# Performance work log

Measured on AMD Instinct MI355X. Metric: run time of the kernel, lower is better.

## Reference

```python
import jax, jax.numpy as jnp
import numpy as np

D = 1024   # embedding_dim
H = 16     # head_num
DH = D // H
STD = 0.02


def setup_inputs() -> dict:
    key = jax.random.key(0)
    ks = jax.random.split(key, 8)
    B, S = 16, 2048
    inp = {
        "hidden_states": jax.random.normal(ks[0], (B, S, D), dtype=jnp.float32),
        "attention_mask": jnp.zeros((B, 1, S), dtype=jnp.float32),
        # nn.Linear params, stored as [in, out] for direct matmul
        "Wq": jax.random.normal(ks[1], (D, D), dtype=jnp.float32) * STD,
        "bq": jnp.zeros((D,), dtype=jnp.float32),
        "Wqa": jax.random.normal(ks[2], (D, H), dtype=jnp.float32) * STD,
        "bqa": jnp.zeros((H,), dtype=jnp.float32),
        "Wk": jax.random.normal(ks[3], (D, D), dtype=jnp.float32) * STD,
        "bk": jnp.zeros((D,), dtype=jnp.float32),
        "Wka": jax.random.normal(ks[4], (D, H), dtype=jnp.float32) * STD,
        "bka": jnp.zeros((H,), dtype=jnp.float32),
        "Wt": jax.random.normal(ks[5], (D, D), dtype=jnp.float32) * STD,
        "bt": jnp.zeros((D,), dtype=jnp.float32),
    }
    return inp


def reference(hidden_states, attention_mask, Wq, bq, Wqa, bqa, Wk, bk, Wka, bka, Wt, bt):
    B, S, _ = hidden_states.shape
    scale = 1.0 / np.sqrt(DH).astype(np.float32)

    mixed_q = hidden_states @ Wq + bq          # [B,S,D]
    mixed_k = hidden_states @ Wk + bk          # [B,S,D]

    # per-head query pooling scores: [B,S,H] -> [B,H,S]
    q_score = jnp.transpose(mixed_q @ Wqa + bqa, (0, 2, 1)) * scale + attention_mask
    q_weight = jax.nn.softmax(q_score, axis=-1)                 # [B,H,S]

    q_layer = mixed_q.reshape(B, S, H, DH).transpose(0, 2, 1, 3)  # [B,H,S,dh]
    pooled_q = jnp.einsum('bhs,bhsd->bhd', q_weight, q_layer)     # [B,H,dh]
    pooled_q_flat = pooled_q.reshape(B, 1, D)                     # [B,1,D] (head-major)

    # elementwise modulate keys with pooled query (broadcast, no repeat)
    mixed_qk = mixed_k * pooled_q_flat                            # [B,S,D]

    qk_score = jnp.transpose(mixed_qk @ Wka + bka, (0, 2, 1)) * scale + attention_mask
    qk_weight = jax.nn.softmax(qk_score, axis=-1)                 # [B,H,S]

    k_layer = mixed_qk.reshape(B, S, H, DH).transpose(0, 2, 1, 3)  # [B,H,S,dh]
    pooled_k = jnp.einsum('bhs,bhsd->bhd', qk_weight, k_layer)     # [B,H,dh]

    weighted = pooled_k[:, :, None, :] * q_layer                   # [B,H,S,dh]
    weighted = weighted.transpose(0, 2, 1, 3).reshape(B, S, D)     # [B,S,D]

    return weighted @ Wt + bt + mixed_q
```

## Files before the change

### kernel.cpp

```cpp
#include <hip/hip_runtime.h>
#include <hip/hip_bf16.h>
#include <stdint.h>

#define D_ 1024
#define H_ 16
#define DH_ 64
#define S_ 2048
#define B_ 16
static constexpr float SCALE = 0.125f;

typedef __bf16 bf16_t;
typedef __bf16 bf16x8 __attribute__((ext_vector_type(8)));
typedef __bf16 bf16x4 __attribute__((ext_vector_type(4)));
typedef float  f32x4  __attribute__((ext_vector_type(4)));

__device__ __forceinline__ void llds16(const void* g, void* l) {
  __builtin_amdgcn_global_load_lds(
      (const __attribute__((address_space(1))) void*)g,
      (__attribute__((address_space(3))) void*)l, 16, 0, 0);
}

__global__ __launch_bounds__(256)
void prep_all(const float* __restrict__ Wq, const float* __restrict__ Wk,
              const float* __restrict__ Wt, const float* __restrict__ Wqa,
              const float* __restrict__ Wka, const float* __restrict__ hs,
              bf16_t* __restrict__ WqT, bf16_t* __restrict__ WkT,
              bf16_t* __restrict__ WtT, bf16_t* __restrict__ WqaT,
              bf16_t* __restrict__ WkaT, bf16_t* __restrict__ hsb) {
  __shared__ bf16_t t[64][65];
  const int z = blockIdx.z;
  const int tid = threadIdx.x;
  if (z < 3) {
    const float* src = (z == 0) ? Wq : (z == 1) ? Wk : Wt;
    bf16_t* dst      = (z == 0) ? WqT : (z == 1) ? WkT : WtT;
    const int n0 = blockIdx.x * 64, k0 = blockIdx.y * 64;
    const int r = tid >> 4, c4 = (tid & 15) * 4;
#pragma unroll
    for (int p = 0; p < 4; ++p) {
      int row = p * 16 + r;
      f32x4 f = *(const f32x4*)&src[(size_t)(k0 + row) * 1024 + n0 + c4];
#pragma unroll
      for (int i = 0; i < 4; ++i) t[row][c4 + i] = (bf16_t)f[i];
    }
    __syncthreads();
#pragma unroll
    for (int p = 0; p < 4; ++p) {
      int row = p * 16 + r;
      bf16x4 v;
#pragma unroll
      for (int i = 0; i < 4; ++i) v[i] = t[c4 + i][row];
      *(bf16x4*)&dst[(size_t)(n0 + row) * 1024 + k0 + c4] = v;
    }
  } else if (z == 3) {
    int g = (blockIdx.y * 16 + blockIdx.x) * 256 + tid;
    if (g < 2048) {
      const float* src = (g < 1024) ? Wqa : Wka;
      bf16_t* dst      = (g < 1024) ? WqaT : WkaT;
      int k = g & 1023;
#pragma unroll
      for (int h = 0; h < H_; ++h) dst[h * 1024 + k] = (bf16_t)src[k * H_ + h];
    }
  } else {
    const int slice = z - 4;
    const int fb = blockIdx.y * 16 + blockIdx.x;
    const size_t tbase = ((size_t)slice * 256 + fb) * 256 + tid;
#pragma unroll
    for (int i = 0; i < 4; ++i) {
      size_t e = (tbase + (size_t)i * 1048576) * 8;
      f32x4 a = *(const f32x4*)&hs[e];
      f32x4 b = *(const f32x4*)&hs[e + 4];
      bf16x8 o;
#pragma unroll
      for (int j = 0; j < 4; ++j) { o[j] = (bf16_t)a[j]; o[4 + j] = (bf16_t)b[j]; }
      *(bf16x8*)&hsb[e] = o;
    }
  }
}

__global__ __launch_bounds__(256, 2)
void gemm_qk(const bf16_t* __restrict__ A, const bf16_t* __restrict__ WqT,
             const bf16_t* __restrict__ WkT, const float* __restrict__ bq,
             const float* __restrict__ bk, bf16_t* __restrict__ mq,
             bf16_t* __restrict__ mk) {
  constexpr int K = 1024, N = 1024;
  __shared__ __align__(16) bf16_t lA[128 * 32];
  __shared__ __align__(16) bf16_t lB[128 * 32];
  __shared__ __align__(16) float est[4][16 * 68];
  const int tid = threadIdx.x;
  const int lane = tid & 63, wid = tid >> 6;
  const int wr = wid >> 1, wc = wid & 1;

  const int wgid = (blockIdx.x & 7) * 512 + (blockIdx.x >> 3);
  const int m0 = (wgid >> 4) * 128;
  const int nsel = wgid & 15;
  const int n0 = (nsel & 7) * 128;
  const bf16_t* BT = (nsel < 8) ? WqT : WkT;
  const float* bias = (nsel < 8) ? bq : bk;
  bf16_t* Cout = (nsel < 8) ? mq : mk;

  const int ar = lane & 15;
  const int kq = lane >> 4;

  int rowc[2], colc[2], dstoff[2];
#pragma unroll
  for (int j = 0; j < 2; ++j) {
    int c = j * 256 + tid;
    int row = c >> 2, s = c & 3;
    rowc[j] = row;
    colc[j] = (((s - (row >> 1)) & 3) << 3);
    dstoff[j] = c * 8;
  }

  f32x4 acc[4][4] = {};

  for (int k0 = 0; k0 < K; k0 += 32) {
#pragma unroll
    for (int j = 0; j < 2; ++j) {
      llds16(BT + (size_t)(n0 + rowc[j]) * K + k0 + colc[j], lB + dstoff[j]);
      llds16(A + (size_t)(m0 + rowc[j]) * K + k0 + colc[j], lA + dstoff[j]);
    }
    __syncthreads();
    bf16x8 af[4], bg[4];
#pragma unroll
    for (int m = 0; m < 4; ++m) {
      int r = wr * 64 + m * 16 + ar;
      af[m] = *(const bf16x8*)&lA[r * 32 + (((kq + (r >> 1)) & 3) << 3)];
    }
#pragma unroll
    for (int n = 0; n < 4; ++n) {
      int r = wc * 64 + n * 16 + ar;
      bg[n] = *(const bf16x8*)&lB[r * 32 + (((kq + (r >> 1)) & 3) << 3)];
    }
#pragma unroll
    for (int m = 0; m < 4; ++m)
#pragma unroll
      for (int n = 0; n < 4; ++n)
        acc[m][n] = __builtin_amdgcn_mfma_f32_16x16x32_bf16(af[m], bg[n], acc[m][n], 0, 0, 0);
    __syncthreads();
  }

  float* st = est[wid];
  const int erow = lane >> 2;
  const int ecol = (lane & 3) * 16;
  const int gcb = n0 + wc * 64;
  const int qrow = (lane >> 4) * 4;
  const int qcol = lane & 15;
  f32x4 bb[4];
#pragma unroll
  for (int q = 0; q < 4; ++q) bb[q] = *(const f32x4*)&bias[gcb + ecol + q * 4];
#pragma unroll
  for (int m = 0; m < 4; ++m) {
#pragma unroll
    for (int n = 0; n < 4; ++n)
#pragma unroll
      for (int j = 0; j < 4; ++j)
        st[(qrow + j) * 68 + n * 16 + qcol] = acc[m][n][j];
    asm volatile("s_waitcnt lgkmcnt(0)" ::: "memory");
    __builtin_amdgcn_sched_barrier(0);
    const int grow = m0 + wr * 64 + m * 16 + erow;
    f32x4 v[4];
#pragma unroll
    for (int q = 0; q < 4; ++q) v[q] = *(f32x4*)&st[erow * 68 + ecol + q * 4];
#pragma unroll
    for (int q = 0; q < 4; ++q)
#pragma unroll
      for (int i = 0; i < 4; ++i) v[q][i] += bb[q][i];
    bf16x8 o0, o1;
#pragma unroll
    for (int i = 0; i < 4; ++i) { o0[i] = (bf16_t)v[0][i]; o0[4 + i] = (bf16_t)v[1][i]; }
#pragma unroll
    for (int i = 0; i < 4; ++i) { o1[i] = (bf16_t)v[2][i]; o1[4 + i] = (bf16_t)v[3][i]; }
    bf16_t* op = Cout + (size_t)grow * N + gcb + ecol;
    *(bf16x8*)&op[0] = o0;
    *(bf16x8*)&op[8] = o1;
  }
}

__global__ __launch_bounds__(256, 2)
void gemm_out(const bf16_t* __restrict__ A, const bf16_t* __restrict__ BT,
              const float* __restrict__ bias, float* __restrict__ Cout,
              const bf16_t* __restrict__ resid, const float* __restrict__ pkA) {
  constexpr int K = 1024, N = 1024;
  __shared__ __align__(16) bf16_t lA[128 * 32];
  __shared__ __align__(16) bf16_t lB[128 * 32];
  __shared__ __align__(16) float est[4][16 * 68];
  const int tid = threadIdx.x;
  const int lane = tid & 63, wid = tid >> 6;
  const int wr = wid >> 1, wc = wid & 1;

  const int wgid = (blockIdx.x & 7) * 256 + (blockIdx.x >> 3);
  const int m0 = (wgid >> 3) * 128;
  const int n0 = (wgid & 7) * 128;
  const int b = m0 / S_;

  const int ar = lane & 15;
  const int kq = lane >> 4;

  int rowc[2], colc[2], dstoff[2];
#pragma unroll
  for (int j = 0; j < 2; ++j) {
    int c = j * 256 + tid;
    int row = c >> 2, s = c & 3;
    rowc[j] = row;
    colc[j] = (((s - (row >> 1)) & 3) << 3);
    dstoff[j] = c * 8;
  }

  f32x4 acc[4][4] = {};

  for (int k0 = 0; k0 < K; k0 += 32) {
#pragma unroll
    for (int j = 0; j < 2; ++j) {
      llds16(BT + (size_t)(n0 + rowc[j]) * K + k0 + colc[j], lB + dstoff[j]);
      bf16x8 v = *(const bf16x8*)(A + (size_t)(m0 + rowc[j]) * K + k0 + colc[j]);
      const float* pkp = pkA + b * D_ + k0 + colc[j];
      f32x4 p0 = *(const f32x4*)pkp;
      f32x4 p1 = *(const f32x4*)(pkp + 4);
      bf16x8 o;
#pragma unroll
      for (int i = 0; i < 4; ++i) {
        o[i]     = (bf16_t)((float)v[i] * p0[i]);
        o[4 + i] = (bf16_t)((float)v[4 + i] * p1[i]);
      }
      *(bf16x8*)&lA[dstoff[j]] = o;
    }
    __syncthreads();
    bf16x8 af[4], bg[4];
#pragma unroll
    for (int m = 0; m < 4; ++m) {
      int r = wr * 64 + m * 16 + ar;
      af[m] = *(const bf16x8*)&lA[r * 32 + (((kq + (r >> 1)) & 3) << 3)];
    }
#pragma unroll
    for (int n = 0; n < 4; ++n) {
      int r = wc * 64 + n * 16 + ar;
      bg[n] = *(const bf16x8*)&lB[r * 32 + (((kq + (r >> 1)) & 3) << 3)];
    }
#pragma unroll
    for (int m = 0; m < 4; ++m)
#pragma unroll
      for (int n = 0; n < 4; ++n)
        acc[m][n] = __builtin_amdgcn_mfma_f32_16x16x32_bf16(af[m], bg[n], acc[m][n], 0, 0, 0);
    __syncthreads();
  }

  float* st = est[wid];
  const int erow = lane >> 2;
  const int ecol = (lane & 3) * 16;
  const int gcb = n0 + wc * 64;
  const int qrow = (lane >> 4) * 4;
  const int qcol = lane & 15;
  f32x4 bb[4];
#pragma unroll
  for (int q = 0; q < 4; ++q) bb[q] = *(const f32x4*)&bias[gcb + ecol + q * 4];
#pragma unroll
  for (int m = 0; m < 4; ++m) {
#pragma unroll
    for (int n = 0; n < 4; ++n)
#pragma unroll
      for (int j = 0; j < 4; ++j)
        st[(qrow + j) * 68 + n * 16 + qcol] = acc[m][n][j];
    asm volatile("s_waitcnt lgkmcnt(0)" ::: "memory");
    __builtin_amdgcn_sched_barrier(0);
    const int grow = m0 + wr * 64 + m * 16 + erow;
    f32x4 v[4];
#pragma unroll
    for (int q = 0; q < 4; ++q) v[q] = *(f32x4*)&st[erow * 68 + ecol + q * 4];
#pragma unroll
    for (int q = 0; q < 4; ++q)
#pragma unroll
      for (int i = 0; i < 4; ++i) v[q][i] += bb[q][i];
    bf16x8 r0 = *(const bf16x8*)&resid[(size_t)grow * N + gcb + ecol];
    bf16x8 r1 = *(const bf16x8*)&resid[(size_t)grow * N + gcb + ecol + 8];
#pragma unroll
    for (int i = 0; i < 4; ++i) { v[0][i] += (float)r0[i]; v[1][i] += (float)r0[4 + i]; }
#pragma unroll
    for (int i = 0; i < 4; ++i) { v[2][i] += (float)r1[i]; v[3][i] += (float)r1[4 + i]; }
    float* op = Cout + (size_t)grow * N + gcb + ecol;
#pragma unroll
    for (int q = 0; q < 4; ++q) *(f32x4*)&op[q * 4] = v[q];
  }
}

template <int PER_B>
__global__ __launch_bounds__(256)
void score_kernel(const bf16_t* __restrict__ X, const bf16_t* __restrict__ WaT,
                  const float* __restrict__ ba, const float* __restrict__ mask,
                  float* __restrict__ scores) {
  const int lane = threadIdx.x & 63, wid = threadIdx.x >> 6;
  const int m0 = blockIdx.x * 64 + wid * 16;
  const int ar = lane & 15, ak = (lane >> 4) * 8;
  const int bb = m0 >> 11;
  const bf16_t* Wb = WaT + (PER_B ? (size_t)bb * H_ * D_ : 0);
  f32x4 acc = {};
  for (int k0 = 0; k0 < D_; k0 += 32) {
    bf16x8 a = *(const bf16x8*)&X[(size_t)(m0 + ar) * D_ + k0 + ak];
    bf16x8 b = *(const bf16x8*)&Wb[(size_t)ar * D_ + k0 + ak];
    acc = __builtin_amdgcn_mfma_f32_16x16x32_bf16(a, b, acc, 0, 0, 0);
  }
  const int h = lane & 15;
  const int srow = m0 + (lane >> 4) * 4;
  const int s0 = srow - bb * S_;
  const float bah = ba[h];
  f32x4 mv = *(const f32x4*)&mask[(size_t)bb * S_ + s0];
  f32x4 outv;
#pragma unroll
  for (int j = 0; j < 4; ++j)
    outv[j] = (acc[j] + bah) * SCALE + mv[j];
  *(f32x4*)&scores[((size_t)(bb * H_ + h)) * S_ + s0] = outv;
}

__global__ __launch_bounds__(256)
void softmax_rows(const float* __restrict__ scores, float* __restrict__ wout) {
  __shared__ float rA[4], rB[4];
  const int tid = threadIdx.x, lane = tid & 63, wid = tid >> 6;
  const float* srow = scores + (size_t)blockIdx.x * S_;
  float* wrow = wout + (size_t)blockIdx.x * S_;
  f32x4 v0 = *(const f32x4*)&srow[tid * 4];
  f32x4 v1 = *(const f32x4*)&srow[1024 + tid * 4];
  float mx = fmaxf(fmaxf(fmaxf(v0[0], v0[1]), fmaxf(v0[2], v0[3])),
                   fmaxf(fmaxf(v1[0], v1[1]), fmaxf(v1[2], v1[3])));
#pragma unroll
  for (int o = 32; o; o >>= 1) mx = fmaxf(mx, __shfl_xor(mx, o));
  if (lane == 0) rA[wid] = mx;
  __syncthreads();
  mx = fmaxf(fmaxf(rA[0], rA[1]), fmaxf(rA[2], rA[3]));
  float sum = 0.f;
#pragma unroll
  for (int i = 0; i < 4; ++i) { v0[i] = __expf(v0[i] - mx); sum += v0[i]; }
#pragma unroll
  for (int i = 0; i < 4; ++i) { v1[i] = __expf(v1[i] - mx); sum += v1[i]; }
#pragma unroll
  for (int o = 32; o; o >>= 1) sum += __shfl_xor(sum, o);
  if (lane == 0) rB[wid] = sum;
  __syncthreads();
  sum = rB[0] + rB[1] + rB[2] + rB[3];
  const float inv = 1.0f / sum;
#pragma unroll
  for (int i = 0; i < 4; ++i) { v0[i] *= inv; v1[i] *= inv; }
  *(f32x4*)&wrow[tid * 4] = v0;
  *(f32x4*)&wrow[1024 + tid * 4] = v1;
}

__global__ __launch_bounds__(256)
void pool_partial(const bf16_t* __restrict__ X, const float* __restrict__ w,
                  float* __restrict__ partials) {
  __shared__ float sm[2][1024];
  const int tid = threadIdx.x;
  const int chunk = blockIdx.x, b = blockIdx.y;
  const int s0 = chunk * 32;
  const int dc = (tid & 127) * 8;
  const int sp = tid >> 7;
  const int h = dc >> 6;
  const float* wrow = w + ((size_t)b * H_ + h) * S_ + s0;
  const bf16_t* Xb = X + ((size_t)b * S_ + s0) * D_ + dc;
  float acc[8] = {};
  for (int s = sp; s < 32; s += 2) {
    bf16x8 xv = *(const bf16x8*)&Xb[(size_t)s * D_];
    float wt = wrow[s];
#pragma unroll
    for (int j = 0; j < 8; ++j) acc[j] += wt * (float)xv[j];
  }
#pragma unroll
  for (int j = 0; j < 8; ++j) sm[sp][dc + j] = acc[j];
  __syncthreads();
  const int d0 = tid * 4;
  f32x4 r;
#pragma unroll
  for (int j = 0; j < 4; ++j) r[j] = sm[0][d0 + j] + sm[1][d0 + j];
  *(f32x4*)&partials[((size_t)chunk * B_ + b) * D_ + d0] = r;
}

template <int MODE>
__global__ __launch_bounds__(256)
void pool_reduce(const float* __restrict__ partials, const float* __restrict__ pq,
                 const bf16_t* __restrict__ WkaT, float* __restrict__ pooled,
                 bf16_t* __restrict__ wka_s) {
  const int idx = blockIdx.x * 256 + threadIdx.x;
  float s = 0.f;
#pragma unroll 8
  for (int c = 0; c < 64; ++c) s += partials[(size_t)c * (B_ * D_) + idx];
  if (MODE == 1) s *= pq[idx];
  pooled[idx] = s;
  if (MODE == 0) {
    const int b = idx >> 10, d = idx & 1023;
#pragma unroll
    for (int h = 0; h < H_; ++h)
      wka_s[((size_t)b * H_ + h) * D_ + d] = (bf16_t)(s * (float)WkaT[h * D_ + d]);
  }
}

extern "C" void kernel_launch(void* const* d_in, const int* in_sizes, int n_in,
                              void* d_out, int out_size, void* d_ws, size_t ws_size,
                              hipStream_t stream) {
  const float* hs   = (const float*)d_in[0];
  const float* mask = (const float*)d_in[1];
  const float* Wq   = (const float*)d_in[2];
  const float* bq   = (const float*)d_in[3];
  const float* Wqa  = (const float*)d_in[4];
  const float* bqa  = (const float*)d_in[5];
  const float* Wk   = (const float*)d_in[6];
  const float* bk   = (const float*)d_in[7];
  const float* Wka  = (const float*)d_in[8];
  const float* bka  = (const float*)d_in[9];
  const float* Wt   = (const float*)d_in[10];
  const float* bt   = (const float*)d_in[11];

  char* ws = (char*)d_ws;
  float*  pq    = (float*)(ws + (64u << 10));
  float*  pk    = (float*)(ws + (128u << 10));
  bf16_t* wka_s = (bf16_t*)(ws + (256u << 10));
  bf16_t* WqaT  = (bf16_t*)(ws + (1u << 20));
  bf16_t* WkaT  = (bf16_t*)(ws + (1u << 20) + 32768);
  bf16_t* WqT   = (bf16_t*)(ws + (2u << 20));
  bf16_t* WkT   = (bf16_t*)(ws + (4u << 20));
  bf16_t* WtT   = (bf16_t*)(ws + (6u << 20));
  bf16_t* hsb   = (bf16_t*)(ws + (8u << 20));
  bf16_t* mq    = (bf16_t*)(ws + (8u << 20) + ((size_t)64 << 20));
  bf16_t* mk    = (bf16_t*)(ws + (8u << 20) + ((size_t)128 << 20));
  float* scores = (float*)(ws + (8u << 20) + ((size_t)192 << 20));
  float* wsm    = (float*)(ws + (8u << 20) + ((size_t)194 << 20));
  float* parts  = (float*)(ws + (8u << 20) + ((size_t)196 << 20));

  prep_all<<<dim3(16, 16, 20), 256, 0, stream>>>(Wq, Wk, Wt, Wqa, Wka, hs,
                                                 WqT, WkT, WtT, WqaT, WkaT, hsb);

  gemm_qk<<<4096, 256, 0, stream>>>(hsb, WqT, WkT, bq, bk, mq, mk);

  score_kernel<0><<<512, 256, 0, stream>>>(mq, WqaT, bqa, mask, scores);
  softmax_rows<<<256, 256, 0, stream>>>(scores, wsm);
  pool_partial<<<dim3(64, 16), 256, 0, stream>>>(mq, wsm, parts);
  pool_reduce<0><<<64, 256, 0, stream>>>(parts, nullptr, WkaT, pq, wka_s);

  score_kernel<1><<<512, 256, 0, stream>>>(mk, wka_s, bka, mask, scores);
  softmax_rows<<<256, 256, 0, stream>>>(scores, wsm);
  pool_partial<<<dim3(64, 16), 256, 0, stream>>>(mk, wsm, parts);
  pool_reduce<1><<<64, 256, 0, stream>>>(parts, pq, nullptr, pk, nullptr);

  gemm_out<<<2048, 256, 0, stream>>>(mq, WtT, bt, (float*)d_out, mq, pk);
}
```

Baseline: 395.9 us.

## Enlarge QK GEMM tiles to 256x256 with double-buffered async LDS pipeline

Rewrites the fused Q/K projection GEMM to use 256x256 output tiles per 512-thread workgroup, with each wave holding a 128x64 accumulator block. The K loop now covers 64 elements per iteration, split into two 32-wide halves, and the next tile is loaded into a second LDS buffer while the current one is being computed, using partial vmcnt waits and raw barriers. MFMA sections are bracketed with s_setprio. The goal is to raise arithmetic intensity and hide global-load latency. In exchange it uses far more LDS and registers, limits occupancy to one workgroup, and launches fewer blocks.

```diff
diff --git a/kernel.cpp b/kernel.cpp
--- a/kernel.cpp
+++ b/kernel.cpp
@@ -77,79 +77,117 @@
   }
 }
 
-__global__ __launch_bounds__(256, 2)
+__global__ __launch_bounds__(512, 1)
 void gemm_qk(const bf16_t* __restrict__ A, const bf16_t* __restrict__ WqT,
              const bf16_t* __restrict__ WkT, const float* __restrict__ bq,
              const float* __restrict__ bk, bf16_t* __restrict__ mq,
              bf16_t* __restrict__ mk) {
   constexpr int K = 1024, N = 1024;
-  __shared__ __align__(16) bf16_t lA[128 * 32];
-  __shared__ __align__(16) bf16_t lB[128 * 32];
-  __shared__ __align__(16) float est[4][16 * 68];
+  __shared__ __align__(16) bf16_t lds[2][2][2][256 * 32];
   const int tid = threadIdx.x;
   const int lane = tid & 63, wid = tid >> 6;
-  const int wr = wid >> 1, wc = wid & 1;
-
-  const int wgid = (blockIdx.x & 7) * 512 + (blockIdx.x >> 3);
-  const int m0 = (wgid >> 4) * 128;
-  const int nsel = wgid & 15;
-  const int n0 = (nsel & 7) * 128;
-  const bf16_t* BT = (nsel < 8) ? WqT : WkT;
-  const float* bias = (nsel < 8) ? bq : bk;
-  bf16_t* Cout = (nsel < 8) ? mq : mk;
+  const int wm = wid >> 2, wn = wid & 3;
+
+  const int wgid = (blockIdx.x & 7) * 128 + (blockIdx.x >> 3);
+  const int m0 = (wgid >> 3) * 256;
+  const int nsel = wgid & 7;
+  const int n0 = (nsel & 3) * 256;
+  const bf16_t* BT = (nsel < 4) ? WqT : WkT;
+  const float* bias = (nsel < 4) ? bq : bk;
+  bf16_t* Cout = (nsel < 4) ? mq : mk;
+
+  int srow[2], scol[2];
+#pragma unroll
+  for (int ld = 0; ld < 2; ++ld) {
+    int c = ld * 512 + tid;
+    srow[ld] = c >> 2;
+    scol[ld] = (((c & 3) - (srow[ld] & 3)) & 3) * 8;
+  }
 
   const int ar = lane & 15;
-  const int kq = lane >> 4;
-
-  int rowc[2], colc[2], dstoff[2];
-#pragma unroll
-  for (int j = 0; j < 2; ++j) {
-    int c = j * 256 + tid;
-    int row = c >> 2, s = c & 3;
-    rowc[j] = row;
-    colc[j] = (((s - (row >> 1)) & 3) << 3);
-    dstoff[j] = c * 8;
-  }
-
-  f32x4 acc[4][4] = {};
-
-  for (int k0 = 0; k0 < K; k0 += 32) {
-#pragma unroll
-    for (int j = 0; j < 2; ++j) {
-      llds16(BT + (size_t)(n0 + rowc[j]) * K + k0 + colc[j], lB + dstoff[j]);
-      llds16(A + (size_t)(m0 + rowc[j]) * K + k0 + colc[j], lA + dstoff[j]);
-    }
-    __syncthreads();
-    bf16x8 af[4], bg[4];
-#pragma unroll
-    for (int m = 0; m < 4; ++m) {
-      int r = wr * 64 + m * 16 + ar;
-      af[m] = *(const bf16x8*)&lA[r * 32 + (((kq + (r >> 1)) & 3) << 3)];
-    }
-#pragma unroll
-    for (int n = 0; n < 4; ++n) {
-      int r = wc * 64 + n * 16 + ar;
-      bg[n] = *(const bf16x8*)&lB[r * 32 + (((kq + (r >> 1)) & 3) << 3)];
-    }
-#pragma unroll
-    for (int m = 0; m < 4; ++m)
-#pragma unroll
-      for (int n = 0; n < 4; ++n)
-        acc[m][n] = __builtin_amdgcn_mfma_f32_16x16x32_bf16(af[m], bg[n], acc[m][n], 0, 0, 0);
-    __syncthreads();
-  }
-
-  float* st = est[wid];
+  const int kc = lane >> 4;
+
+  f32x4 acc[8][4] = {};
+
+#define STAGE_(MAT, KH, KOFF, NXT)                                             \
+  {                                                                            \
+    const bf16_t* srcb = (MAT == 0) ? A : BT;                                  \
+    const int rb = (MAT == 0) ? m0 : n0;                                       \
+    _Pragma("unroll")                                                          \
+    for (int ld = 0; ld < 2; ++ld) {                                           \
+      llds16(srcb + (size_t)(rb + srow[ld]) * K + (KOFF) + (KH) * 32 + scol[ld], \
+             &lds[NXT][MAT][KH][(ld * 512 + tid) * 8]);                        \
+    }                                                                          \
+  }
+
+#define COMPUTE_(KH, MH, CUR)                                                  \
+  {                                                                            \
+    bf16x8 af[4], bg[4];                                                       \
+    _Pragma("unroll")                                                          \
+    for (int mm = 0; mm < 4; ++mm) {                                           \
+      int r = wm * 128 + ((MH) * 4 + mm) * 16 + ar;                            \
+      int slot = (kc + (r & 3)) & 3;                                           \
+      af[mm] = *(const bf16x8*)&lds[CUR][0][KH][r * 32 + slot * 8];            \
+    }                                                                          \
+    _Pragma("unroll")                                                          \
+    for (int nn = 0; nn < 4; ++nn) {                                           \
+      int r = wn * 64 + nn * 16 + ar;                                          \
+      int slot = (kc + (r & 3)) & 3;                                           \
+      bg[nn] = *(const bf16x8*)&lds[CUR][1][KH][r * 32 + slot * 8];            \
+    }                                                                          \
+    __builtin_amdgcn_s_setprio(1);                                             \
+    _Pragma("unroll")                                                          \
+    for (int mm = 0; mm < 4; ++mm)                                             \
+      _Pragma("unroll")                                                        \
+      for (int nn = 0; nn < 4; ++nn)                                           \
+        acc[(MH) * 4 + mm][nn] = __builtin_amdgcn_mfma_f32_16x16x32_bf16(      \
+            af[mm], bg[nn], acc[(MH) * 4 + mm][nn], 0, 0, 0);                  \
+    __builtin_amdgcn_s_setprio(0);                                             \
+  }
+
+  STAGE_(0, 0, 0, 0); STAGE_(1, 0, 0, 0); STAGE_(0, 1, 0, 0); STAGE_(1, 1, 0, 0);
+
+#pragma unroll 1
+  for (int t = 0; t < 15; ++t) {
+    const int cur = t & 1, nxt = cur ^ 1;
+    const int koff = (t + 1) * 64;
+    STAGE_(0, 0, koff, nxt);
+    asm volatile("s_waitcnt vmcnt(6)" ::: "memory");
+    __builtin_amdgcn_s_barrier();
+    COMPUTE_(0, 0, cur);
+    STAGE_(1, 0, koff, nxt);
+    COMPUTE_(0, 1, cur);
+    STAGE_(0, 1, koff, nxt);
+    asm volatile("s_waitcnt vmcnt(6)" ::: "memory");
+    __builtin_amdgcn_s_barrier();
+    COMPUTE_(1, 0, cur);
+    STAGE_(1, 1, koff, nxt);
+    COMPUTE_(1, 1, cur);
+  }
+  asm volatile("s_waitcnt vmcnt(4)" ::: "memory");
+  __builtin_amdgcn_s_barrier();
+  COMPUTE_(0, 0, 1);
+  COMPUTE_(0, 1, 1);
+  asm volatile("s_waitcnt vmcnt(0)" ::: "memory");
+  __builtin_amdgcn_s_barrier();
+  COMPUTE_(1, 0, 1);
+  COMPUTE_(1, 1, 1);
+#undef STAGE_
+#undef COMPUTE_
+
+  __syncthreads();
+
+  float* st = (float*)&lds[0][0][0][0] + wid * (16 * 68);
   const int erow = lane >> 2;
   const int ecol = (lane & 3) * 16;
-  const int gcb = n0 + wc * 64;
+  const int gcb = n0 + wn * 64;
   const int qrow = (lane >> 4) * 4;
   const int qcol = lane & 15;
   f32x4 bb[4];
 #pragma unroll
   for (int q = 0; q < 4; ++q) bb[q] = *(const f32x4*)&bias[gcb + ecol + q * 4];
 #pragma unroll
-  for (int m = 0; m < 4; ++m) {
+  for (int m = 0; m < 8; ++m) {
 #pragma unroll
     for (int n = 0; n < 4; ++n)
 #pragma unroll
@@ -157,7 +195,7 @@
         st[(qrow + j) * 68 + n * 16 + qcol] = acc[m][n][j];
     asm volatile("s_waitcnt lgkmcnt(0)" ::: "memory");
     __builtin_amdgcn_sched_barrier(0);
-    const int grow = m0 + wr * 64 + m * 16 + erow;
+    const int grow = m0 + wm * 128 + m * 16 + erow;
     f32x4 v[4];
 #pragma unroll
     for (int q = 0; q < 4; ++q) v[q] = *(f32x4*)&st[erow * 68 + ecol + q * 4];
@@ -425,7 +463,7 @@
   prep_all<<<dim3(16, 16, 20), 256, 0, stream>>>(Wq, Wk, Wt, Wqa, Wka, hs,
                                                  WqT, WkT, WtT, WqaT, WkaT, hsb);
 
-  gemm_qk<<<4096, 256, 0, stream>>>(hsb, WqT, WkT, bq, bk, mq, mk);
+  gemm_qk<<<1024, 512, 0, stream>>>(hsb, WqT, WkT, bq, bk, mq, mk);
 
   score_kernel<0><<<512, 256, 0, stream>>>(mq, WqaT, bqa, mask, scores);
   softmax_rows<<<256, 256, 0, stream>>>(scores, wsm);
```

New measurement: 365.4 us. 7.7% less time.
